# Optimization experiments

Hardware: AMD Instinct MI355X
Metric: run time of the kernel (lower is better)

Reference implementation:

```python
import jax, jax.numpy as jnp
import numpy as np

B, N, C, Q, H, RATIO = 8, 8700, 256, 300, 8, 4
D = C // H
HID = C * RATIO
EPS = 1e-5


def _ln(x, w, b):
    m = jnp.mean(x, axis=-1, keepdims=True)
    v = jnp.mean((x - m) ** 2, axis=-1, keepdims=True)
    return (x - m) * jax.lax.rsqrt(v + EPS) * w + b


def setup_inputs() -> dict:
    key = jax.random.key(0)
    ks = jax.random.split(key, 8)
    s = 0.02
    return {
        "x": jax.random.normal(ks[0], (B, N, C), jnp.float32),
        # linear weights stored [in, out] (y = x @ W), no biases (qkv_bias=False, Mlp bias=False)
        "Wq": jax.random.normal(ks[1], (C, C), jnp.float32) * s,
        "Wk": jax.random.normal(ks[2], (C, C), jnp.float32) * s,
        "Wv": jax.random.normal(ks[3], (C, C), jnp.float32) * s,
        "Wp": jax.random.normal(ks[4], (C, C), jnp.float32) * s,
        "W1": jax.random.normal(ks[5], (C, HID), jnp.float32) * s,
        "W2": jax.random.normal(ks[6], (HID, C), jnp.float32) * s,
        "ln1_w": jnp.ones((C,), jnp.float32),
        "ln1_b": jnp.zeros((C,), jnp.float32),
        "ln2_w": jnp.ones((C,), jnp.float32),
        "ln2_b": jnp.zeros((C,), jnp.float32),
        "gamma1": jnp.ones((C,), jnp.float32),
        "gamma2": jnp.ones((C,), jnp.float32),
    }


def reference(x, Wq, Wk, Wv, Wp, W1, W2, ln1_w, ln1_b, ln2_w, ln2_b, gamma1, gamma2):
    scale = D ** -0.5
    xn = _ln(x, ln1_w, ln1_b)                       # [B,N,C]
    # SAQAttn: queries only from the first Q tokens; keys/values from all N tokens
    q = (xn[:, :Q] @ Wq).reshape(B, Q, H, D) * scale  # [B,Q,H,D]
    k = (xn @ Wk).reshape(B, N, H, D)
    v = (xn @ Wv).reshape(B, N, H, D)
    attn = jax.nn.softmax(jnp.einsum('bqhd,bnhd->bhqn', q, k), axis=-1)  # [B,H,Q,N]
    x_det = jnp.einsum('bhqn,bnhd->bqhd', attn, v).reshape(B, Q, C) @ Wp  # [B,Q,C]
    # residual with layer-scale gamma1; context tokens pass normed features through
    x_attn = jnp.concatenate([x_det, xn[:, Q:]], axis=1)
    x = x + gamma1 * x_attn
    # tokens_norm=False: norm2 only on query tokens
    x = jnp.concatenate([_ln(x[:, :Q], ln2_w, ln2_b), x[:, Q:]], axis=1)
    # MLP on query tokens with layer-scale gamma2 (exact GELU, as nn.GELU default)
    det = gamma2 * (jax.nn.gelu(x[:, :Q] @ W1, approximate=False) @ W2)
    # faithful to source: x_res + cat([det, x[:,Q:]]) doubles the context tokens
    return x + jnp.concatenate([det, x[:, Q:]], axis=1)
```

## Files before the change

### kernel.cpp

```cpp
#include <hip/hip_runtime.h>

#define BB 8
#define NN 8700
#define CC 256
#define QQ 300
#define HH 8
#define DD 32
#define HIDN 1024
#define NSPLIT 20
#define TSTR (NSPLIT * 64)
#define KSLACK 1536

typedef unsigned short u16;
typedef __attribute__((ext_vector_type(8))) short short8;
typedef __attribute__((ext_vector_type(4))) float f32x4;

#define MFMA16(a, b, c) __builtin_amdgcn_mfma_f32_16x16x32_bf16((a), (b), (c), 0, 0, 0)

__device__ __forceinline__ u16 f2bu(float f) {
    unsigned int u = __builtin_bit_cast(unsigned int, f);
    u += 0x7fffu + ((u >> 16) & 1u);
    return (u16)(u >> 16);
}
__device__ __forceinline__ unsigned int cvtpk(float lo, float hi) {
    unsigned int r;
    asm("v_cvt_pk_bf16_f32 %0, %1, %2" : "=v"(r) : "v"(lo), "v"(hi));
    return r;
}
__device__ __forceinline__ void gload16(const u16* g, u16* l) {
    __builtin_amdgcn_global_load_lds(
        (const __attribute__((address_space(1))) void*)g,
        (__attribute__((address_space(3))) void*)l, 16, 0, 0);
}

__global__ __launch_bounds__(256)
void wprep_t(const float* __restrict__ Wq, const float* __restrict__ Wk,
             const float* __restrict__ Wv, const float* __restrict__ Wp,
             const float* __restrict__ W1, const float* __restrict__ W2,
             u16* __restrict__ dst, float qscale)
{
    __shared__ u16 tl[64][66];
    int bid = blockIdx.x;
    const float* src; int K, N, tr, tc; size_t dof; float sc = 1.f;
    if (bid < 64) {
        int mat = bid >> 4, ti = bid & 15;
        src = (mat == 0) ? Wq : (mat == 1) ? Wk : (mat == 2) ? Wv : Wp;
        K = 256; N = 256; tr = ti >> 2; tc = ti & 3;
        dof = (size_t)mat * 65536;
        if (mat == 0) sc = qscale;
    } else if (bid < 128) {
        int ti = bid - 64; src = W1; K = 256; N = 1024; tr = ti >> 4; tc = ti & 15; dof = 262144;
    } else {
        int ti = bid - 128; src = W2; K = 1024; N = 256; tr = ti >> 2; tc = ti & 3; dof = 524288;
    }
    int tid = threadIdx.x;
    int jj = tid & 63;
    int i0 = tid >> 6;
#pragma unroll
    for (int ii = 0; ii < 16; ii++) {
        int kk = i0 * 16 + ii;
        float v = src[(size_t)(tr * 64 + kk) * N + tc * 64 + jj] * sc;
        tl[kk][jj] = f2bu(v);
    }
    __syncthreads();
#pragma unroll
    for (int ii = 0; ii < 16; ii++) {
        int nn = i0 * 16 + ii;
        dst[dof + (size_t)(tc * 64 + nn) * K + tr * 64 + jj] = tl[jj][nn];
    }
}

__global__ __launch_bounds__(256)
void ln1_k(const float* __restrict__ x, const float* __restrict__ w,
           const float* __restrict__ bv, const float* __restrict__ g1,
           u16* __restrict__ xn, float* __restrict__ out)
{
    int row = blockIdx.x * 4 + (threadIdx.x >> 6);
    int l = threadIdx.x & 63;
    size_t base = (size_t)row * CC + l * 4;
    float4 xv = *reinterpret_cast<const float4*>(x + base);
    float s  = xv.x + xv.y + xv.z + xv.w;
    float s2 = xv.x * xv.x + xv.y * xv.y + xv.z * xv.z + xv.w * xv.w;
#pragma unroll
    for (int m = 1; m < 64; m <<= 1) {
        s  += __shfl_xor(s,  m, 64);
        s2 += __shfl_xor(s2, m, 64);
    }
    float mean = s * (1.0f / CC);
    float rs = rsqrtf(s2 * (1.0f / CC) - mean * mean + 1e-5f);
    float4 wv = *reinterpret_cast<const float4*>(w  + l * 4);
    float4 bb = *reinterpret_cast<const float4*>(bv + l * 4);
    float n0 = (xv.x - mean) * rs * wv.x + bb.x;
    float n1 = (xv.y - mean) * rs * wv.y + bb.y;
    float n2 = (xv.z - mean) * rs * wv.z + bb.z;
    float n3 = (xv.w - mean) * rs * wv.w + bb.w;
    ushort4 u; u.x = f2bu(n0); u.y = f2bu(n1); u.z = f2bu(n2); u.w = f2bu(n3);
    *reinterpret_cast<ushort4*>(xn + base) = u;
    int n = row % NN;
    if (n >= QQ) {
        float4 gv = *reinterpret_cast<const float4*>(g1 + l * 4);
        float4 o;
        o.x = 2.0f * (xv.x + gv.x * n0);
        o.y = 2.0f * (xv.y + gv.y * n1);
        o.z = 2.0f * (xv.z + gv.z * n2);
        o.w = 2.0f * (xv.w + gv.w * n3);
        *reinterpret_cast<float4*>(out + base) = o;
    }
}

__global__ __launch_bounds__(256)
void ln2_k(const float* __restrict__ x, const float* __restrict__ pd,
           const float* __restrict__ g1, const float* __restrict__ w,
           const float* __restrict__ bv, float* __restrict__ xqf, u16* __restrict__ xqb)
{
    int r = blockIdx.x * 4 + (threadIdx.x >> 6);
    int l = threadIdx.x & 63;
    int b = r / QQ, n = r - b * QQ;
    size_t xoff = ((size_t)b * NN + n) * CC + l * 4;
    size_t roff = (size_t)r * CC + l * 4;
    float4 xv = *reinterpret_cast<const float4*>(x + xoff);
    float4 pv = *reinterpret_cast<const float4*>(pd + roff);
    float4 gv = *reinterpret_cast<const float4*>(g1 + l * 4);
    float x0 = xv.x + gv.x * pv.x;
    float x1 = xv.y + gv.y * pv.y;
    float x2 = xv.z + gv.z * pv.z;
    float x3 = xv.w + gv.w * pv.w;
    float s  = x0 + x1 + x2 + x3;
    float s2 = x0 * x0 + x1 * x1 + x2 * x2 + x3 * x3;
#pragma unroll
    for (int m = 1; m < 64; m <<= 1) {
        s  += __shfl_xor(s,  m, 64);
        s2 += __shfl_xor(s2, m, 64);
    }
    float mean = s * (1.0f / CC);
    float rs = rsqrtf(s2 * (1.0f / CC) - mean * mean + 1e-5f);
    float4 wv = *reinterpret_cast<const float4*>(w  + l * 4);
    float4 bb = *reinterpret_cast<const float4*>(bv + l * 4);
    float n0 = (x0 - mean) * rs * wv.x + bb.x;
    float n1 = (x1 - mean) * rs * wv.y + bb.y;
    float n2 = (x2 - mean) * rs * wv.z + bb.z;
    float n3 = (x3 - mean) * rs * wv.w + bb.w;
    float4 o; o.x = n0; o.y = n1; o.z = n2; o.w = n3;
    *reinterpret_cast<float4*>(xqf + roff) = o;
    ushort4 u; u.x = f2bu(n0); u.y = f2bu(n1); u.z = f2bu(n2); u.w = f2bu(n3);
    *reinterpret_cast<ushort4*>(xqb + roff) = u;
}

__global__ __launch_bounds__(512)
void gemm_kv(const u16* __restrict__ A, const u16* __restrict__ WT,
             u16* __restrict__ Cb, u16* __restrict__ Cb2, int M)
{
    __shared__ u16 alds[64 * 256];
    const int tid = threadIdx.x;
    const int w = tid >> 6, l = tid & 63;
    const int l15 = l & 15, kg = l >> 4;
    const int rowbase = blockIdx.x * 64;
    const f32x4 fz = {0.f, 0.f, 0.f, 0.f};

    {
        const char* gb = (const char*)(A + (size_t)rowbase * CC);
        char* lb = (char*)alds;
#pragma unroll
        for (int j = 0; j < 4; j++) {
            int o = tid * 64 + j * 16;
            short8 v = *reinterpret_cast<const short8*>(gb + o);
            int d = o ^ (((o >> 9) & 7) << 4);
            *reinterpret_cast<short8*>(lb + d) = v;
        }
    }
    __syncthreads();

    const int colbase = w * 64;
    const u16* bp[4];
#pragma unroll
    for (int ni = 0; ni < 4; ni++)
        bp[ni] = WT + (size_t)(colbase + ni * 16 + l15) * CC + kg * 8;

    f32x4 acc[4][4];
#pragma unroll
    for (int mi = 0; mi < 4; mi++)
#pragma unroll
        for (int ni = 0; ni < 4; ni++) acc[mi][ni] = fz;

    const char* lb = (const char*)alds;
    const int sw = (l15 & 7) << 4;
    int abase[4];
#pragma unroll
    for (int mi = 0; mi < 4; mi++) abase[mi] = (mi * 16 + l15) << 9;

#pragma unroll
    for (int ks = 0; ks < 8; ks++) {
        const int koff = ((ks * 64) + (kg * 16)) ^ sw;
        short8 a[4], bfr[4];
#pragma unroll
        for (int mi = 0; mi < 4; mi++)
            a[mi] = *reinterpret_cast<const short8*>(lb + abase[mi] + koff);
#pragma unroll
        for (int ni = 0; ni < 4; ni++)
            bfr[ni] = *reinterpret_cast<const short8*>(bp[ni] + ks * 32);
#pragma unroll
        for (int mi = 0; mi < 4; mi++)
#pragma unroll
            for (int ni = 0; ni < 4; ni++)
                acc[mi][ni] = MFMA16(a[mi], bfr[ni], acc[mi][ni]);
    }

#pragma unroll
    for (int mi = 0; mi < 4; mi++) {
#pragma unroll
        for (int j = 0; j < 4; j++) {
            int r = rowbase + mi * 16 + kg * 4 + j;
            if (r >= M) continue;
#pragma unroll
            for (int ni = 0; ni < 4; ni++) {
                int col = colbase + ni * 16 + l15;
                float v = acc[mi][ni][j];
                if (col < CC) Cb[(size_t)r * CC + col] = f2bu(v);
                else          Cb2[(size_t)r * CC + (col - CC)] = f2bu(v);
            }
        }
    }
}

template<int EPI, int MT>
__global__ __launch_bounds__(256)
void gemm_k(const u16* __restrict__ A, const u16* __restrict__ WT,
            u16* __restrict__ Cb, u16* __restrict__ Cb2, float* __restrict__ Cf,
            const float* __restrict__ basep, const float* __restrict__ gvec,
            float* __restrict__ outp,
            int M, int K, int ldC, int rpb, int bstr)
{
    constexpr int NM = MT / 16;
    const int w = threadIdx.x >> 6, l = threadIdx.x & 63;
    const int l15 = l & 15, kg = l >> 4;
    const int rowbase = blockIdx.x * MT;
    const int colbase = blockIdx.y * 256 + w * 64;
    const short8 z8 = {0, 0, 0, 0, 0, 0, 0, 0};
    const f32x4 fz = {0.f, 0.f, 0.f, 0.f};

    const u16* ap[NM]; bool av[NM];
#pragma unroll
    for (int mi = 0; mi < NM; mi++) {
        int r = rowbase + mi * 16 + l15;
        av[mi] = (r < M);
        int rr = av[mi] ? r : 0;
        size_t ar = (size_t)(rr / rpb) * bstr + (rr % rpb);
        ap[mi] = A + ar * K + kg * 8;
    }
    const u16* bp[4];
#pragma unroll
    for (int ni = 0; ni < 4; ni++) {
        int col = colbase + ni * 16 + l15;
        bp[ni] = WT + (size_t)col * K + kg * 8;
    }
    f32x4 acc[NM][4];
#pragma unroll
    for (int mi = 0; mi < NM; mi++)
#pragma unroll
        for (int ni = 0; ni < 4; ni++) acc[mi][ni] = fz;

    for (int ks = 0; ks < K; ks += 32) {
        short8 a[NM], bfr[4];
#pragma unroll
        for (int mi = 0; mi < NM; mi++)
            a[mi] = av[mi] ? *reinterpret_cast<const short8*>(ap[mi] + ks) : z8;
#pragma unroll
        for (int ni = 0; ni < 4; ni++)
            bfr[ni] = *reinterpret_cast<const short8*>(bp[ni] + ks);
#pragma unroll
        for (int mi = 0; mi < NM; mi++)
#pragma unroll
            for (int ni = 0; ni < 4; ni++)
                acc[mi][ni] = MFMA16(a[mi], bfr[ni], acc[mi][ni]);
    }
#pragma unroll
    for (int mi = 0; mi < NM; mi++) {
#pragma unroll
        for (int j = 0; j < 4; j++) {
            int r = rowbase + mi * 16 + kg * 4 + j;
            if (r >= M) continue;
#pragma unroll
            for (int ni = 0; ni < 4; ni++) {
                int col = colbase + ni * 16 + l15;
                float v = acc[mi][ni][j];
                if (EPI == 0) {
                    if (col < CC) Cb[(size_t)r * ldC + col] = f2bu(v);
                    else          Cb2[(size_t)r * ldC + (col - CC)] = f2bu(v);
                } else if (EPI == 1) {
                    float gl = 0.5f * v * (1.0f + erff(v * 0.70710678118654752f));
                    Cb[(size_t)r * ldC + col] = f2bu(gl);
                } else if (EPI == 2) {
                    Cf[(size_t)r * ldC + col] = v;
                } else {
                    float res = basep[(size_t)r * CC + col] + gvec[col] * v;
                    size_t orow = (size_t)(r / QQ) * NN + (r % QQ);
                    outp[orow * CC + col] = res;
                }
            }
        }
    }
}

__global__ __launch_bounds__(256)
void attn_k(const u16* __restrict__ qm, const u16* __restrict__ km,
            const u16* __restrict__ vm, float* __restrict__ Op,
            float* __restrict__ lp)
{
    __shared__ u16 klds[2][64 * 32];
    __shared__ u16 vt[2][32 * 64];
    __shared__ u16 plds[4][2][16 * 64];

    const int bx = blockIdx.x;
    const int split = bx >> 6;
    const int rem = bx & 63;
    const int h = rem >> 3, b = rem & 7;
    const int bh = b * HH + h;
    const int tid = threadIdx.x;
    const int w = tid >> 6, l = tid & 63;
    const int l15 = l & 15, kg = l >> 4;
    const int tstart = split * 64;
    const int nt = (NN - tstart + TSTR - 1) / TSTR;

    const f32x4 fz = {0.f, 0.f, 0.f, 0.f};
    const short os = (short)0x3F80;
    const short8 ones = {os, os, os, os, os, os, os, os};

    const u16* kbase = km + (size_t)b * NN * CC + h * DD;
    const u16* vbase = vm + (size_t)b * NN * CC + h * DD;
    const int vkp = (tid & 31) * 2;
    const int vdg = (tid >> 5) * 4;

    const int krow  = (w << 4) + (l >> 2);
    const int kslot = (l & 3) ^ ((krow >> 1) & 3);
    const u16* ksrc = kbase + (size_t)krow * CC + kslot * 8;

    short8 qfr[5];
#pragma unroll
    for (int qf = 0; qf < 5; qf++) {
        int qrow = w * 80 + qf * 16 + l15;
        int qc = qrow < QQ ? qrow : 0;
        qfr[qf] = *reinterpret_cast<const short8*>(qm + ((size_t)(b * QQ + qc) * CC + h * DD + kg * 8));
    }

    f32x4 o[2][5]; float lpart[5];
#pragma unroll
    for (int qf = 0; qf < 5; qf++) { o[0][qf] = fz; o[1][qf] = fz; lpart[qf] = 0.f; }

    gload16(ksrc + (size_t)tstart * CC, (u16*)((char*)klds[0] + (w << 10)));
    ushort4 v0r = *reinterpret_cast<const ushort4*>(vbase + (size_t)(tstart + vkp) * CC + vdg);
    ushort4 v1r = *reinterpret_cast<const ushort4*>(vbase + (size_t)(tstart + vkp + 1) * CC + vdg);

    char* pl = (char*)plds[w];
    const int rdswz = ((l15 << 7) ^ ((l15 & 7) << 4)) + (kg << 4);
    const int wrbase = (l15 << 7) ^ ((l15 & 7) << 4);

    for (int t = 0; t < nt; ++t) {
        const int n0 = tstart + t * TSTR;
        char* vtb = (char*)vt[t & 1];
#pragma unroll
        for (int i = 0; i < 4; i++) {
            int row = vdg + i;
            unsigned int pk2 = (unsigned int)v0r[i] | ((unsigned int)v1r[i] << 16);
            int byteo = ((row << 7) + (vkp << 1)) ^ ((row & 7) << 4);
            *reinterpret_cast<unsigned int*>(vtb + byteo) = pk2;
        }
        __syncthreads();

        gload16(ksrc + (size_t)(n0 + TSTR) * CC, (u16*)((char*)klds[(t + 1) & 1] + (w << 10)));
        ushort4 v0n = *reinterpret_cast<const ushort4*>(vbase + (size_t)(n0 + TSTR + vkp) * CC + vdg);
        ushort4 v1n = *reinterpret_cast<const ushort4*>(vbase + (size_t)(n0 + TSTR + vkp + 1) * CC + vdg);

        short8 kf[4];
        { const char* klb = (const char*)klds[t & 1];
#pragma unroll
          for (int kb = 0; kb < 4; kb++) {
              int row = kb * 16 + l15;
              int off = (row << 6) + ((kg ^ ((row >> 1) & 3)) << 4);
              kf[kb] = *reinterpret_cast<const short8*>(klb + off);
          } }

        short8 va[2][2];
#pragma unroll
        for (int ks = 0; ks < 2; ks++)
#pragma unroll
            for (int dg = 0; dg < 2; dg++) {
                int row = dg * 16 + l15;
                int byteo = ((row << 7) + 64 * ks + 16 * kg) ^ ((row & 7) << 4);
                va[ks][dg] = *reinterpret_cast<const short8*>(vtb + byteo);
            }

        const bool tail = (n0 + 64 > NN);

#pragma unroll
        for (int qf = 0; qf < 5; qf++) {
            short8 bp0, bp1;
            if (qf > 0) {
                const char* plr = pl + (((qf - 1) & 1) << 11);
                bp0 = *reinterpret_cast<const short8*>(plr + rdswz);
                bp1 = *reinterpret_cast<const short8*>(plr + rdswz + 64);
            }
            f32x4 s[4];
            __builtin_amdgcn_s_setprio(1);
#pragma unroll
            for (int kb = 0; kb < 4; kb++)
                s[kb] = MFMA16(kf[kb], qfr[qf], fz);
            __builtin_amdgcn_s_setprio(0);
            char* plw = pl + ((qf & 1) << 11);
#pragma unroll
            for (int kb = 0; kb < 4; kb++) {
                float p0 = exp2f(s[kb][0]);
                float p1 = exp2f(s[kb][1]);
                float p2 = exp2f(s[kb][2]);
                float p3 = exp2f(s[kb][3]);
                if (tail) {
                    int kbase2 = n0 + 16 * kb + 4 * kg;
                    if (kbase2 + 0 >= NN) p0 = 0.f;
                    if (kbase2 + 1 >= NN) p1 = 0.f;
                    if (kbase2 + 2 >= NN) p2 = 0.f;
                    if (kbase2 + 3 >= NN) p3 = 0.f;
                }
                int byte0 = wrbase + ((16 * kb + 4 * kg) << 1);
                *reinterpret_cast<unsigned int*>(plw + byte0)     = cvtpk(p0, p1);
                *reinterpret_cast<unsigned int*>(plw + byte0 + 4) = cvtpk(p2, p3);
            }
            if (qf > 0) {
                __builtin_amdgcn_s_setprio(1);
                o[0][qf - 1] = MFMA16(va[0][0], bp0, o[0][qf - 1]);
                o[1][qf - 1] = MFMA16(va[0][1], bp0, o[1][qf - 1]);
                o[0][qf - 1] = MFMA16(va[1][0], bp1, o[0][qf - 1]);
                o[1][qf - 1] = MFMA16(va[1][1], bp1, o[1][qf - 1]);
                f32x4 tsum = MFMA16(ones, bp0, fz);
                tsum = MFMA16(ones, bp1, tsum);
                __builtin_amdgcn_s_setprio(0);
                lpart[qf - 1] += tsum[0];
            }
        }
        {
            const char* plr = pl + 0;
            short8 bp0 = *reinterpret_cast<const short8*>(plr + rdswz);
            short8 bp1 = *reinterpret_cast<const short8*>(plr + rdswz + 64);
            __builtin_amdgcn_s_setprio(1);
            o[0][4] = MFMA16(va[0][0], bp0, o[0][4]);
            o[1][4] = MFMA16(va[0][1], bp0, o[1][4]);
            o[0][4] = MFMA16(va[1][0], bp1, o[0][4]);
            o[1][4] = MFMA16(va[1][1], bp1, o[1][4]);
            f32x4 tsum = MFMA16(ones, bp0, fz);
            tsum = MFMA16(ones, bp1, tsum);
            __builtin_amdgcn_s_setprio(0);
            lpart[4] += tsum[0];
        }
        v0r = v0n; v1r = v1n;
    }

    size_t pb = (size_t)(split * 64 + bh) * QQ;
#pragma unroll
    for (int qf = 0; qf < 5; qf++) {
        int q = w * 80 + qf * 16 + l15;
        if (q >= QQ) continue;
        size_t pr = pb + q;
        if (kg == 0) lp[pr] = lpart[qf];
        *reinterpret_cast<f32x4*>(Op + pr * DD + kg * 4)      = o[0][qf];
        *reinterpret_cast<f32x4*>(Op + pr * DD + 16 + kg * 4) = o[1][qf];
    }
}

__global__ __launch_bounds__(256)
void comb_k(const float* __restrict__ Op, const float* __restrict__ lp, u16* __restrict__ ao)
{
    int g = blockIdx.x * 256 + threadIdx.x;
    int d4 = (g & 7) * 4;
    int row = g >> 3;
    int bh = row / QQ, qq = row - bh * QQ;
    int b = bh >> 3, h = bh & 7;
    float L = 0.f, a0 = 0.f, a1 = 0.f, a2 = 0.f, a3 = 0.f;
#pragma unroll
    for (int s = 0; s < NSPLIT; s++) {
        size_t pr = (size_t)(s * 64 + bh) * QQ + qq;
        L += lp[pr];
        float4 ov = *reinterpret_cast<const float4*>(Op + pr * DD + d4);
        a0 += ov.x; a1 += ov.y; a2 += ov.z; a3 += ov.w;
    }
    float inv = 1.0f / L;
    ushort4 u;
    u.x = f2bu(a0 * inv); u.y = f2bu(a1 * inv); u.z = f2bu(a2 * inv); u.w = f2bu(a3 * inv);
    *reinterpret_cast<ushort4*>(ao + ((size_t)(b * QQ + qq) * CC + h * DD + d4)) = u;
}

extern "C" void kernel_launch(void* const* d_in, const int* in_sizes, int n_in,
                              void* d_out, int out_size, void* d_ws, size_t ws_size,
                              hipStream_t stream)
{
    (void)in_sizes; (void)n_in; (void)out_size; (void)ws_size;
    const float* x    = (const float*)d_in[0];
    const float* Wq   = (const float*)d_in[1];
    const float* Wk   = (const float*)d_in[2];
    const float* Wv   = (const float*)d_in[3];
    const float* Wp   = (const float*)d_in[4];
    const float* W1   = (const float*)d_in[5];
    const float* W2   = (const float*)d_in[6];
    const float* ln1w = (const float*)d_in[7];
    const float* ln1b = (const float*)d_in[8];
    const float* ln2w = (const float*)d_in[9];
    const float* ln2b = (const float*)d_in[10];
    const float* g1   = (const float*)d_in[11];
    const float* g2   = (const float*)d_in[12];
    float* out = (float*)d_out;

    char* p = (char*)d_ws;
    auto alloc = [&](size_t bytes) { char* r = p; p += (bytes + 255) & ~(size_t)255; return r; };

    const size_t MKV = (size_t)BB * NN;
    const size_t MQ  = (size_t)BB * QQ;

    u16* WqT  = (u16*)alloc((size_t)CC * CC * 2);
    u16* WkvT = (u16*)alloc((size_t)CC * CC * 2 * 2);
    u16* WpT  = (u16*)alloc((size_t)CC * CC * 2);
    u16* W1T  = (u16*)alloc((size_t)CC * HIDN * 2);
    u16* W2T  = (u16*)alloc((size_t)HIDN * CC * 2);
    u16* xn   = (u16*)alloc((MKV + 64) * CC * 2);
    u16* kbf  = (u16*)alloc((MKV + KSLACK) * CC * 2);
    u16* vbf  = (u16*)alloc((MKV + KSLACK) * CC * 2);
    u16* qbf  = (u16*)alloc(MQ * CC * 2);
    u16* aob  = (u16*)alloc(MQ * CC * 2);
    u16* xqb  = (u16*)alloc(MQ * CC * 2);
    u16* h1   = (u16*)alloc(MQ * HIDN * 2);
    float* pd  = (float*)alloc(MQ * CC * 4);
    float* xqf = (float*)alloc(MQ * CC * 4);
    float* Op  = (float*)alloc((size_t)NSPLIT * 64 * QQ * DD * 4);
    float* lp  = (float*)alloc((size_t)NSPLIT * 64 * QQ * 4);

    const float qscale = 0.17677669529663687f * 1.4426950408889634f;

    wprep_t<<<192, 256, 0, stream>>>(Wq, Wk, Wv, Wp, W1, W2, WqT, qscale);

    ln1_k<<<(int)(MKV / 4), 256, 0, stream>>>(x, ln1w, ln1b, g1, xn, out);

    gemm_kv<<<1088, 512, 0, stream>>>(xn, WkvT, kbf, vbf, (int)MKV);
    gemm_k<0, 16><<<dim3(150, 1), 256, 0, stream>>>(xn, WqT, qbf, nullptr, nullptr, nullptr, nullptr, nullptr,
                                                    (int)MQ, CC, CC, QQ, NN);

    attn_k<<<64 * NSPLIT, 256, 0, stream>>>(qbf, kbf, vbf, Op, lp);
    comb_k<<<(int)(MQ * 8 / 256), 256, 0, stream>>>(Op, lp, aob);

    gemm_k<2, 16><<<dim3(150, 1), 256, 0, stream>>>(aob, WpT, nullptr, nullptr, pd, nullptr, nullptr, nullptr,
                                                    (int)MQ, CC, CC, (int)MQ, 0);
    ln2_k<<<(int)(MQ / 4), 256, 0, stream>>>(x, pd, g1, ln2w, ln2b, xqf, xqb);

    gemm_k<1, 16><<<dim3(150, 4), 256, 0, stream>>>(xqb, W1T, h1, nullptr, nullptr, nullptr, nullptr, nullptr,
                                                    (int)MQ, CC, HIDN, (int)MQ, 0);
    gemm_k<3, 16><<<dim3(150, 1), 256, 0, stream>>>(h1, W2T, nullptr, nullptr, nullptr, xqf, g2, out,
                                                    (int)MQ, HIDN, CC, (int)MQ, 0);
}
```

Before: 228.1 us.

## Vectorize GEMM epilogues via swapped MFMA operands, store attention partials as bf16

Swaps the MFMA A/B operands so each lane holds four consecutive output columns, which lets the GEMM epilogues write packed uint2/float4 stores instead of scalar ones. Replaces software bf16 rounding with the hardware v_cvt_pk_bf16_f32 instruction throughout. Stores the split-attention partial outputs as bf16 instead of fp32, halving that intermediate traffic, and lowers NSPLIT from 20 to 16. The bf16 partials lose some precision in the combine step, and the smaller split count reduces the number of attention blocks.

```diff
diff --git a/kernel.cpp b/kernel.cpp
--- a/kernel.cpp
+++ b/kernel.cpp
@@ -7,7 +7,7 @@
 #define HH 8
 #define DD 32
 #define HIDN 1024
-#define NSPLIT 20
+#define NSPLIT 16
 #define TSTR (NSPLIT * 64)
 #define KSLACK 1536
 
@@ -17,15 +17,15 @@
 
 #define MFMA16(a, b, c) __builtin_amdgcn_mfma_f32_16x16x32_bf16((a), (b), (c), 0, 0, 0)
 
-__device__ __forceinline__ u16 f2bu(float f) {
-    unsigned int u = __builtin_bit_cast(unsigned int, f);
-    u += 0x7fffu + ((u >> 16) & 1u);
-    return (u16)(u >> 16);
-}
 __device__ __forceinline__ unsigned int cvtpk(float lo, float hi) {
     unsigned int r;
     asm("v_cvt_pk_bf16_f32 %0, %1, %2" : "=v"(r) : "v"(lo), "v"(hi));
     return r;
+}
+__device__ __forceinline__ u16 f2b_hw(float f) { return (u16)cvtpk(f, 0.f); }
+__device__ __forceinline__ float b2f(u16 u) {
+    unsigned int x = ((unsigned int)u) << 16;
+    return __builtin_bit_cast(float, x);
 }
 __device__ __forceinline__ void gload16(const u16* g, u16* l) {
     __builtin_amdgcn_global_load_lds(
@@ -60,7 +60,7 @@
     for (int ii = 0; ii < 16; ii++) {
         int kk = i0 * 16 + ii;
         float v = src[(size_t)(tr * 64 + kk) * N + tc * 64 + jj] * sc;
-        tl[kk][jj] = f2bu(v);
+        tl[kk][jj] = f2b_hw(v);
     }
     __syncthreads();
 #pragma unroll
@@ -94,8 +94,8 @@
     float n1 = (xv.y - mean) * rs * wv.y + bb.y;
     float n2 = (xv.z - mean) * rs * wv.z + bb.z;
     float n3 = (xv.w - mean) * rs * wv.w + bb.w;
-    ushort4 u; u.x = f2bu(n0); u.y = f2bu(n1); u.z = f2bu(n2); u.w = f2bu(n3);
-    *reinterpret_cast<ushort4*>(xn + base) = u;
+    uint2 u; u.x = cvtpk(n0, n1); u.y = cvtpk(n2, n3);
+    *reinterpret_cast<uint2*>(xn + base) = u;
     int n = row % NN;
     if (n >= QQ) {
         float4 gv = *reinterpret_cast<const float4*>(g1 + l * 4);
@@ -142,8 +142,8 @@
     float n3 = (x3 - mean) * rs * wv.w + bb.w;
     float4 o; o.x = n0; o.y = n1; o.z = n2; o.w = n3;
     *reinterpret_cast<float4*>(xqf + roff) = o;
-    ushort4 u; u.x = f2bu(n0); u.y = f2bu(n1); u.z = f2bu(n2); u.w = f2bu(n3);
-    *reinterpret_cast<ushort4*>(xqb + roff) = u;
+    uint2 u; u.x = cvtpk(n0, n1); u.y = cvtpk(n2, n3);
+    *reinterpret_cast<uint2*>(xqb + roff) = u;
 }
 
 __global__ __launch_bounds__(512)
@@ -202,22 +202,20 @@
         for (int mi = 0; mi < 4; mi++)
 #pragma unroll
             for (int ni = 0; ni < 4; ni++)
-                acc[mi][ni] = MFMA16(a[mi], bfr[ni], acc[mi][ni]);
+                acc[mi][ni] = MFMA16(bfr[ni], a[mi], acc[mi][ni]);
     }
 
 #pragma unroll
     for (int mi = 0; mi < 4; mi++) {
-#pragma unroll
-        for (int j = 0; j < 4; j++) {
-            int r = rowbase + mi * 16 + kg * 4 + j;
-            if (r >= M) continue;
-#pragma unroll
-            for (int ni = 0; ni < 4; ni++) {
-                int col = colbase + ni * 16 + l15;
-                float v = acc[mi][ni][j];
-                if (col < CC) Cb[(size_t)r * CC + col] = f2bu(v);
-                else          Cb2[(size_t)r * CC + (col - CC)] = f2bu(v);
-            }
+        int r = rowbase + mi * 16 + l15;
+        if (r >= M) continue;
+#pragma unroll
+        for (int ni = 0; ni < 4; ni++) {
+            int col0 = colbase + ni * 16 + kg * 4;
+            f32x4 v = acc[mi][ni];
+            uint2 pk; pk.x = cvtpk(v[0], v[1]); pk.y = cvtpk(v[2], v[3]);
+            if (col0 < CC) *reinterpret_cast<uint2*>(Cb  + (size_t)r * CC + col0)        = pk;
+            else           *reinterpret_cast<uint2*>(Cb2 + (size_t)r * CC + (col0 - CC)) = pk;
         }
     }
 }
@@ -271,31 +269,40 @@
         for (int mi = 0; mi < NM; mi++)
 #pragma unroll
             for (int ni = 0; ni < 4; ni++)
-                acc[mi][ni] = MFMA16(a[mi], bfr[ni], acc[mi][ni]);
+                acc[mi][ni] = MFMA16(bfr[ni], a[mi], acc[mi][ni]);
     }
 #pragma unroll
     for (int mi = 0; mi < NM; mi++) {
-#pragma unroll
-        for (int j = 0; j < 4; j++) {
-            int r = rowbase + mi * 16 + kg * 4 + j;
-            if (r >= M) continue;
-#pragma unroll
-            for (int ni = 0; ni < 4; ni++) {
-                int col = colbase + ni * 16 + l15;
-                float v = acc[mi][ni][j];
-                if (EPI == 0) {
-                    if (col < CC) Cb[(size_t)r * ldC + col] = f2bu(v);
-                    else          Cb2[(size_t)r * ldC + (col - CC)] = f2bu(v);
-                } else if (EPI == 1) {
-                    float gl = 0.5f * v * (1.0f + erff(v * 0.70710678118654752f));
-                    Cb[(size_t)r * ldC + col] = f2bu(gl);
-                } else if (EPI == 2) {
-                    Cf[(size_t)r * ldC + col] = v;
-                } else {
-                    float res = basep[(size_t)r * CC + col] + gvec[col] * v;
-                    size_t orow = (size_t)(r / QQ) * NN + (r % QQ);
-                    outp[orow * CC + col] = res;
-                }
+        int r = rowbase + mi * 16 + l15;
+        if (r >= M) continue;
+#pragma unroll
+        for (int ni = 0; ni < 4; ni++) {
+            int col0 = colbase + ni * 16 + kg * 4;
+            f32x4 v = acc[mi][ni];
+            if (EPI == 0) {
+                uint2 pk; pk.x = cvtpk(v[0], v[1]); pk.y = cvtpk(v[2], v[3]);
+                if (col0 < CC) *reinterpret_cast<uint2*>(Cb  + (size_t)r * ldC + col0)        = pk;
+                else           *reinterpret_cast<uint2*>(Cb2 + (size_t)r * ldC + (col0 - CC)) = pk;
+            } else if (EPI == 1) {
+                float g0 = 0.5f * v[0] * (1.0f + erff(v[0] * 0.70710678118654752f));
+                float g1 = 0.5f * v[1] * (1.0f + erff(v[1] * 0.70710678118654752f));
+                float g2 = 0.5f * v[2] * (1.0f + erff(v[2] * 0.70710678118654752f));
+                float g3 = 0.5f * v[3] * (1.0f + erff(v[3] * 0.70710678118654752f));
+                uint2 pk; pk.x = cvtpk(g0, g1); pk.y = cvtpk(g2, g3);
+                *reinterpret_cast<uint2*>(Cb + (size_t)r * ldC + col0) = pk;
+            } else if (EPI == 2) {
+                float4 o; o.x = v[0]; o.y = v[1]; o.z = v[2]; o.w = v[3];
+                *reinterpret_cast<float4*>(Cf + (size_t)r * ldC + col0) = o;
+            } else {
+                float4 xv = *reinterpret_cast<const float4*>(basep + (size_t)r * CC + col0);
+                float4 gv = *reinterpret_cast<const float4*>(gvec + col0);
+                float4 o;
+                o.x = xv.x + gv.x * v[0];
+                o.y = xv.y + gv.y * v[1];
+                o.z = xv.z + gv.z * v[2];
+                o.w = xv.w + gv.w * v[3];
+                size_t orow = (size_t)(r / QQ) * NN + (r % QQ);
+                *reinterpret_cast<float4*>(outp + orow * CC + col0) = o;
             }
         }
     }
@@ -303,7 +310,7 @@
 
 __global__ __launch_bounds__(256)
 void attn_k(const u16* __restrict__ qm, const u16* __restrict__ km,
-            const u16* __restrict__ vm, float* __restrict__ Op,
+            const u16* __restrict__ vm, u16* __restrict__ Opb,
             float* __restrict__ lp)
 {
     __shared__ u16 klds[2][64 * 32];
@@ -419,9 +426,8 @@
                     if (kbase2 + 2 >= NN) p2 = 0.f;
                     if (kbase2 + 3 >= NN) p3 = 0.f;
                 }
-                int byte0 = wrbase + ((16 * kb + 4 * kg) << 1);
-                *reinterpret_cast<unsigned int*>(plw + byte0)     = cvtpk(p0, p1);
-                *reinterpret_cast<unsigned int*>(plw + byte0 + 4) = cvtpk(p2, p3);
+                uint2 pw; pw.x = cvtpk(p0, p1); pw.y = cvtpk(p2, p3);
+                *reinterpret_cast<uint2*>(plw + (wrbase + ((16 * kb + 4 * kg) << 1))) = pw;
             }
             if (qf > 0) {
                 __builtin_amdgcn_s_setprio(1);
@@ -459,13 +465,15 @@
         if (q >= QQ) continue;
         size_t pr = pb + q;
         if (kg == 0) lp[pr] = lpart[qf];
-        *reinterpret_cast<f32x4*>(Op + pr * DD + kg * 4)      = o[0][qf];
-        *reinterpret_cast<f32x4*>(Op + pr * DD + 16 + kg * 4) = o[1][qf];
+        uint2 w0; w0.x = cvtpk(o[0][qf][0], o[0][qf][1]); w0.y = cvtpk(o[0][qf][2], o[0][qf][3]);
+        uint2 w1; w1.x = cvtpk(o[1][qf][0], o[1][qf][1]); w1.y = cvtpk(o[1][qf][2], o[1][qf][3]);
+        *reinterpret_cast<uint2*>(Opb + pr * DD + kg * 4)      = w0;
+        *reinterpret_cast<uint2*>(Opb + pr * DD + 16 + kg * 4) = w1;
     }
 }
 
 __global__ __launch_bounds__(256)
-void comb_k(const float* __restrict__ Op, const float* __restrict__ lp, u16* __restrict__ ao)
+void comb_k(const u16* __restrict__ Opb, const float* __restrict__ lp, u16* __restrict__ ao)
 {
     int g = blockIdx.x * 256 + threadIdx.x;
     int d4 = (g & 7) * 4;
@@ -477,13 +485,12 @@
     for (int s = 0; s < NSPLIT; s++) {
         size_t pr = (size_t)(s * 64 + bh) * QQ + qq;
         L += lp[pr];
-        float4 ov = *reinterpret_cast<const float4*>(Op + pr * DD + d4);
-        a0 += ov.x; a1 += ov.y; a2 += ov.z; a3 += ov.w;
+        ushort4 ov = *reinterpret_cast<const ushort4*>(Opb + pr * DD + d4);
+        a0 += b2f(ov.x); a1 += b2f(ov.y); a2 += b2f(ov.z); a3 += b2f(ov.w);
     }
     float inv = 1.0f / L;
-    ushort4 u;
-    u.x = f2bu(a0 * inv); u.y = f2bu(a1 * inv); u.z = f2bu(a2 * inv); u.w = f2bu(a3 * inv);
-    *reinterpret_cast<ushort4*>(ao + ((size_t)(b * QQ + qq) * CC + h * DD + d4)) = u;
+    uint2 u; u.x = cvtpk(a0 * inv, a1 * inv); u.y = cvtpk(a2 * inv, a3 * inv);
+    *reinterpret_cast<uint2*>(ao + ((size_t)(b * QQ + qq) * CC + h * DD + d4)) = u;
 }
 
 extern "C" void kernel_launch(void* const* d_in, const int* in_sizes, int n_in,
@@ -526,7 +533,7 @@
     u16* h1   = (u16*)alloc(MQ * HIDN * 2);
     float* pd  = (float*)alloc(MQ * CC * 4);
     float* xqf = (float*)alloc(MQ * CC * 4);
-    float* Op  = (float*)alloc((size_t)NSPLIT * 64 * QQ * DD * 4);
+    u16* Opb  = (u16*)alloc((size_t)NSPLIT * 64 * QQ * DD * 2);
     float* lp  = (float*)alloc((size_t)NSPLIT * 64 * QQ * 4);
 
     const float qscale = 0.17677669529663687f * 1.4426950408889634f;
@@ -539,8 +546,8 @@
     gemm_k<0, 16><<<dim3(150, 1), 256, 0, stream>>>(xn, WqT, qbf, nullptr, nullptr, nullptr, nullptr, nullptr,
                                                     (int)MQ, CC, CC, QQ, NN);
 
-    attn_k<<<64 * NSPLIT, 256, 0, stream>>>(qbf, kbf, vbf, Op, lp);
-    comb_k<<<(int)(MQ * 8 / 256), 256, 0, stream>>>(Op, lp, aob);
+    attn_k<<<64 * NSPLIT, 256, 0, stream>>>(qbf, kbf, vbf, Opb, lp);
+    comb_k<<<(int)(MQ * 8 / 256), 256, 0, stream>>>(Opb, lp, aob);
 
     gemm_k<2, 16><<<dim3(150, 1), 256, 0, stream>>>(aob, WpT, nullptr, nullptr, pd, nullptr, nullptr, nullptr,
                                                     (int)MQ, CC, CC, (int)MQ, 0);
```

Result: faster. 223.4 us (-2.0%).
